# Performance work log

Measured on AMD Instinct MI355X. Metric: run time of the kernel, lower is better.

The kernel has to match this reference:

```python
import jax, jax.numpy as jnp
import numpy as np

D_MODEL = 1024
NHEAD = 16
HEAD_DIM = D_MODEL // NHEAD
EPS = 1e-5


def layer_norm(x, gamma, beta):
    mu = jnp.mean(x, axis=-1, keepdims=True)
    var = jnp.mean(jnp.square(x - mu), axis=-1, keepdims=True)
    return (x - mu) * jax.lax.rsqrt(var + EPS) * gamma + beta


def setup_inputs() -> dict:
    key = jax.random.key(0)
    ks = jax.random.split(key, 12)
    d = D_MODEL
    s = 1.0 / np.sqrt(d)
    return {
        "x": jax.random.normal(ks[0], (4, 2048, d), dtype=jnp.float32),
        "wq": jax.random.normal(ks[1], (d, d), dtype=jnp.float32) * s,
        "wk": jax.random.normal(ks[2], (d, d), dtype=jnp.float32) * s,
        "wv": jax.random.normal(ks[3], (d, d), dtype=jnp.float32) * s,
        "wo": jax.random.normal(ks[4], (d, d), dtype=jnp.float32) * s,
        "bo": jnp.zeros((d,), dtype=jnp.float32),
        "gx": jnp.ones((d,), dtype=jnp.float32),
        "bx": jnp.zeros((d,), dtype=jnp.float32),
        "gf": jnp.ones((d,), dtype=jnp.float32),
        "bf": jnp.zeros((d,), dtype=jnp.float32),
        "w1": jax.random.normal(ks[5], (d, d), dtype=jnp.float32) * s,
        "b1": jnp.zeros((d,), dtype=jnp.float32),
        "w2": jax.random.normal(ks[6], (d, d), dtype=jnp.float32) * s,
        "b2": jnp.zeros((d,), dtype=jnp.float32),
    }


def reference(x, wq, wk, wv, wo, bo, gx, bx, gf, bf, w1, b1, w2, b2):
    B, S, D = x.shape
    H, Dh = NHEAD, HEAD_DIM
    xs = layer_norm(x, gx, bx)
    q = (xs @ wq).reshape(B, S, H, Dh)
    k = (xs @ wk).reshape(B, S, H, Dh)
    v = (xs @ wv).reshape(B, S, H, Dh)
    scores = jnp.einsum("bqhd,bkhd->bhqk", q, k) / jnp.sqrt(jnp.float32(Dh))
    attn = jax.nn.softmax(scores, axis=-1)  # dropout p=0 -> identity
    o = jnp.einsum("bhqk,bkhd->bqhd", attn, v).reshape(B, S, D)
    attn_out = o @ wo + bo
    xt = x + attn_out
    h = layer_norm(xt, gf, bf)
    ffn = jax.nn.relu(h @ w1 + b1) @ w2 + b2
    return xt + ffn
```

## Files before the change

### kernel.cpp

```cpp
#include <hip/hip_runtime.h>
#include <hip/hip_bf16.h>

typedef __bf16 bf16;
typedef bf16 bf16x8 __attribute__((ext_vector_type(8)));
typedef bf16 bf16x4 __attribute__((ext_vector_type(4)));
typedef float f32x4 __attribute__((ext_vector_type(4)));
typedef float f32x16 __attribute__((ext_vector_type(16)));

#define AS1 __attribute__((address_space(1)))
#define AS3 __attribute__((address_space(3)))

static constexpr int SEQ = 2048;
static constexpr int NH  = 16;
static constexpr int DH  = 64;
static constexpr float SCLQ = 0.125f * 1.44269504088896340736f;

__device__ __forceinline__ void gload16(const void* g, void* l) {
  __builtin_amdgcn_global_load_lds((const AS1 void*)g, (AS3 void*)l, 16, 0, 0);
}

__device__ __forceinline__ unsigned pk2(float a, float b) {
  union { bf16 h[2]; unsigned u; } z;
  z.h[0] = (bf16)a; z.h[1] = (bf16)b;
  return z.u;
}

__device__ __forceinline__ void plswap(unsigned &a, unsigned &b) {
  asm volatile("v_permlane32_swap_b32 %0, %1" : "+v"(a), "+v"(b));
}

__global__ __launch_bounds__(256) void prep_w(
    const float* __restrict__ w0, const float* __restrict__ w1,
    const float* __restrict__ w2, const float* __restrict__ w3,
    const float* __restrict__ w4, const float* __restrict__ w5,
    bf16* __restrict__ dst)
{
  __shared__ float tile[64][65];
  int bid = blockIdx.x;
  int wi = bid >> 8;
  int tl = bid & 255;
  int tk = (tl >> 4) << 6;
  int tn = (tl & 15) << 6;
  const float* W = w0;
  if (wi == 1) W = w1; else if (wi == 2) W = w2; else if (wi == 3) W = w3;
  else if (wi == 4) W = w4; else if (wi == 5) W = w5;
  int t = threadIdx.x;
  #pragma unroll
  for (int rep = 0; rep < 16; ++rep) {
    int idx = rep * 256 + t;
    int i = idx >> 6, j = idx & 63;
    tile[i][j] = W[(size_t)(tk + i) * 1024 + tn + j];
  }
  __syncthreads();
  bf16* out = dst + (size_t)wi * 1024 * 1024;
  #pragma unroll
  for (int rep = 0; rep < 16; ++rep) {
    int idx = rep * 256 + t;
    int i = idx >> 6, j = idx & 63;
    out[(size_t)(tn + i) * 1024 + tk + j] = (bf16)tile[j][i];
  }
}

__global__ __launch_bounds__(256) void ln_k(
    const float* __restrict__ x, const float* __restrict__ g,
    const float* __restrict__ bb, bf16* __restrict__ out)
{
  int row = blockIdx.x;
  int t = threadIdx.x;
  float4 v = ((const float4*)(x + (size_t)row * 1024))[t];
  float s  = v.x + v.y + v.z + v.w;
  float s2 = v.x * v.x + v.y * v.y + v.z * v.z + v.w * v.w;
  #pragma unroll
  for (int m = 1; m < 64; m <<= 1) { s += __shfl_xor(s, m); s2 += __shfl_xor(s2, m); }
  __shared__ float red[8];
  int w = t >> 6;
  if ((t & 63) == 0) { red[w] = s; red[4 + w] = s2; }
  __syncthreads();
  s  = red[0] + red[1] + red[2] + red[3];
  s2 = red[4] + red[5] + red[6] + red[7];
  float mu  = s * (1.0f / 1024.0f);
  float var = s2 * (1.0f / 1024.0f) - mu * mu;
  float rst = rsqrtf(var + 1e-5f);
  float4 gv = ((const float4*)g)[t];
  float4 bv = ((const float4*)bb)[t];
  bf16x4 o;
  o[0] = (bf16)((v.x - mu) * rst * gv.x + bv.x);
  o[1] = (bf16)((v.y - mu) * rst * gv.y + bv.y);
  o[2] = (bf16)((v.z - mu) * rst * gv.z + bv.z);
  o[3] = (bf16)((v.w - mu) * rst * gv.w + bv.w);
  *(bf16x4*)(out + (size_t)row * 1024 + t * 4) = o;
}

template<int EPI, int NT>
__global__ __launch_bounds__(256) void gemm_k(
    const bf16* __restrict__ A, const bf16* __restrict__ Bt,
    const float* __restrict__ bias, const float* __restrict__ res,
    float* __restrict__ outf, bf16* __restrict__ outb)
{
  __shared__ bf16 lA[128 * 64];
  __shared__ bf16 lB[128 * 64];
  int t = threadIdx.x;
  int wg = blockIdx.x;
  int swz = (wg & 7) * (NT * 8) + (wg >> 3);
  int mt = swz / NT, nt = swz % NT;
  int lane = t & 63, w = t >> 6;
  int l16 = lane & 15, lh = lane >> 4;
  int wr = w >> 1, wc = w & 1;

  f32x4 acc[4][4] = {};
  const size_t mbase = (size_t)mt * 128;
  const size_t nbase = (size_t)nt * 128;
  int u = t & 7;

  for (int ks = 0; ks < 16; ++ks) {
    int k0 = ks * 64;
    #pragma unroll
    for (int i = 0; i < 4; ++i) {
      int row = i * 32 + (t >> 3);
      int up = u ^ (row & 7);
      gload16(A  + (mbase + row) * 1024 + k0 + up * 8, lA + i * 2048 + w * 512);
      gload16(Bt + (nbase + row) * 1024 + k0 + up * 8, lB + i * 2048 + w * 512);
    }
    __syncthreads();
    #pragma unroll
    for (int kc = 0; kc < 2; ++kc) {
      bf16x8 af[4], bfr[4];
      #pragma unroll
      for (int mi = 0; mi < 4; ++mi) {
        int row = wr * 64 + mi * 16 + l16;
        af[mi] = *(const bf16x8*)(lA + row * 64 + (((kc * 4 + lh) ^ (row & 7)) * 8));
      }
      #pragma unroll
      for (int ni = 0; ni < 4; ++ni) {
        int row = wc * 64 + ni * 16 + l16;
        bfr[ni] = *(const bf16x8*)(lB + row * 64 + (((kc * 4 + lh) ^ (row & 7)) * 8));
      }
      #pragma unroll
      for (int mi = 0; mi < 4; ++mi)
        #pragma unroll
        for (int ni = 0; ni < 4; ++ni)
          acc[mi][ni] = __builtin_amdgcn_mfma_f32_16x16x32_bf16(af[mi], bfr[ni], acc[mi][ni], 0, 0, 0);
    }
    __syncthreads();
  }

  int mrow0 = mt * 128 + wr * 64;
  int ncol0 = nt * 128 + wc * 64;
  #pragma unroll
  for (int mi = 0; mi < 4; ++mi) {
    #pragma unroll
    for (int ni = 0; ni < 4; ++ni) {
      if constexpr (EPI == 0) {
        int gcol = ncol0 + ni * 16 + l16;
        int which = gcol >> 10;
        int col = gcol & 1023;
        int h = col >> 6, dh = col & 63;
        bf16* dst = outb + (size_t)which * (size_t)(4 * NH * SEQ * DH);
        if (which == 2) {
          int s0 = mrow0 + mi * 16 + lh * 4;
          int b = s0 >> 11, s = s0 & 2047;
          bf16x4 pkv;
          #pragma unroll
          for (int r = 0; r < 4; ++r) pkv[r] = (bf16)acc[mi][ni][r];
          *(bf16x4*)(dst + (((size_t)((b * NH + h) * DH + dh)) << 11) + s) = pkv;
        } else {
          #pragma unroll
          for (int r = 0; r < 4; ++r) {
            int grow = mrow0 + mi * 16 + lh * 4 + r;
            int b = grow >> 11, s = grow & 2047;
            float v = acc[mi][ni][r];
            if (which == 0) v *= SCLQ;
            dst[(((size_t)((b * NH + h) * SEQ + s)) << 6) + dh] = (bf16)v;
          }
        }
      } else {
        #pragma unroll
        for (int r = 0; r < 4; ++r) {
          int grow = mrow0 + mi * 16 + lh * 4 + r;
          int gcol = ncol0 + ni * 16 + l16;
          float v = acc[mi][ni][r];
          if constexpr (EPI == 2) {
            size_t idx = (size_t)grow * 1024 + gcol;
            outf[idx] = v + bias[gcol] + res[idx];
          } else {
            size_t idx = (size_t)grow * 1024 + gcol;
            float z = v + bias[gcol];
            outb[idx] = (bf16)(z > 0.f ? z : 0.f);
          }
        }
      }
    }
  }
}

__global__ __launch_bounds__(256) void attn_k(
    const bf16* __restrict__ q, const bf16* __restrict__ kk,
    const bf16* __restrict__ vt, bf16* __restrict__ o)
{
  __shared__ bf16 lK[2][4096];
  __shared__ bf16 lV[2][4096];

  int t = threadIdx.x;
  int lane = t & 63, w = t >> 6;
  int l31 = lane & 31, hi = lane >> 5;
  int bid = blockIdx.x;
  int swz = (bid & 7) * 128 + (bid >> 3);
  int bh = swz >> 4, qt = swz & 15;
  int q0 = qt * 128 + w * 32;
  size_t bhS = (size_t)bh * SEQ;

  const bf16* qrow = q + (bhS + q0 + l31) * 64 + hi * 8;
  bf16x8 aq[4];
  #pragma unroll
  for (int ks = 0; ks < 4; ++ks) aq[ks] = *(const bf16x8*)(qrow + ks * 16);

  int srow = t >> 3;
  int u8 = (t & 7) ^ (srow & 7);
  const bf16* kSrc = kk + (bhS + srow) * 64 + u8 * 8;
  const bf16* vSrc = vt + ((size_t)bh * 64 + srow) * SEQ + u8 * 8;

  f32x16 oacc[2] = {};
  float lsum = 0.f;

  gload16(kSrc,            &lK[0][w * 512]);
  gload16(kSrc + 2048,     &lK[0][2048 + w * 512]);
  gload16(vSrc,            &lV[0][w * 512]);
  gload16(vSrc + 32 * SEQ, &lV[0][2048 + w * 512]);
  __syncthreads();

  #pragma unroll 2
  for (int kt = 0; kt < 32; ++kt) {
    const int cur = kt & 1;
    if (kt < 31) {
      const bf16* ks2 = kSrc + (size_t)(kt + 1) * 4096;
      const bf16* vs2 = vSrc + (kt + 1) * 64;
      gload16(ks2,            &lK[cur ^ 1][w * 512]);
      gload16(ks2 + 2048,     &lK[cur ^ 1][2048 + w * 512]);
      gload16(vs2,            &lV[cur ^ 1][w * 512]);
      gload16(vs2 + 32 * SEQ, &lV[cur ^ 1][2048 + w * 512]);
    }

    const bf16* bK = &lK[cur][0];
    const bf16* bV = &lV[cur][0];

    f32x16 sA = {}, sB = {};
    __builtin_amdgcn_s_setprio(1);
    #pragma unroll
    for (int ks = 0; ks < 4; ++ks) {
      int u = ((2 * ks + hi) ^ (l31 & 7)) * 8;
      bf16x8 k0 = *(const bf16x8*)(bK + l31 * 64 + u);
      bf16x8 k1 = *(const bf16x8*)(bK + (32 + l31) * 64 + u);
      sA = __builtin_amdgcn_mfma_f32_32x32x16_bf16(k0, aq[ks], sA, 0, 0, 0);
      sB = __builtin_amdgcn_mfma_f32_32x32x16_bf16(k1, aq[ks], sB, 0, 0, 0);
    }
    __builtin_amdgcn_s_setprio(0);

    float p[32];
    #pragma unroll
    for (int i = 0; i < 16; ++i) {
      p[i]      = __builtin_amdgcn_exp2f(sA[i]);
      p[16 + i] = __builtin_amdgcn_exp2f(sB[i]);
    }

    float t8[8];
    #pragma unroll
    for (int i = 0; i < 8; ++i)
      t8[i] = (p[4 * i] + p[4 * i + 1]) + (p[4 * i + 2] + p[4 * i + 3]);
    lsum += ((t8[0] + t8[1]) + (t8[2] + t8[3])) + ((t8[4] + t8[5]) + (t8[6] + t8[7]));

    __builtin_amdgcn_s_setprio(1);
    #pragma unroll
    for (int ks = 0; ks < 4; ++ks) {
      int g = 8 * ks;
      unsigned X0 = pk2(p[g],     p[g + 1]), X1 = pk2(p[g + 2], p[g + 3]);
      unsigned Y0 = pk2(p[g + 4], p[g + 5]), Y1 = pk2(p[g + 6], p[g + 7]);
      plswap(X0, Y0);
      plswap(X1, Y1);
      union { unsigned u[4]; bf16x8 v; } cv;
      cv.u[0] = X0; cv.u[1] = X1; cv.u[2] = Y0; cv.u[3] = Y1;
      int u = ((2 * ks + hi) ^ (l31 & 7)) * 8;
      bf16x8 v0 = *(const bf16x8*)(bV + l31 * 64 + u);
      bf16x8 v1 = *(const bf16x8*)(bV + (32 + l31) * 64 + u);
      oacc[0] = __builtin_amdgcn_mfma_f32_32x32x16_bf16(cv.v, v0, oacc[0], 0, 0, 0);
      oacc[1] = __builtin_amdgcn_mfma_f32_32x32x16_bf16(cv.v, v1, oacc[1], 0, 0, 0);
    }
    __builtin_amdgcn_s_setprio(0);

    __syncthreads();
  }

  lsum += __shfl_xor(lsum, 32);
  float inv = 1.0f / lsum;
  int bb = bh >> 4, hh = bh & 15;
  size_t obase = ((size_t)bb * SEQ + q0) * 1024 + (size_t)hh * 64;
  #pragma unroll
  for (int r = 0; r < 16; ++r) {
    int qrw = (r & 3) + 8 * (r >> 2) + 4 * hi;
    float iv = __shfl(inv, qrw);
    size_t base = obase + (size_t)qrw * 1024;
    o[base + l31]      = (bf16)(oacc[0][r] * iv);
    o[base + 32 + l31] = (bf16)(oacc[1][r] * iv);
  }
}

extern "C" void kernel_launch(void* const* d_in, const int* in_sizes, int n_in,
                              void* d_out, int out_size, void* d_ws, size_t ws_size,
                              hipStream_t stream) {
  const float* x   = (const float*)d_in[0];
  const float* wq  = (const float*)d_in[1];
  const float* wk  = (const float*)d_in[2];
  const float* wv  = (const float*)d_in[3];
  const float* wo  = (const float*)d_in[4];
  const float* bo  = (const float*)d_in[5];
  const float* gx  = (const float*)d_in[6];
  const float* bx  = (const float*)d_in[7];
  const float* gf  = (const float*)d_in[8];
  const float* bfp = (const float*)d_in[9];
  const float* w1  = (const float*)d_in[10];
  const float* b1  = (const float*)d_in[11];
  const float* w2  = (const float*)d_in[12];
  const float* b2  = (const float*)d_in[13];

  char* ws = (char*)d_ws;
  const size_t MB = 1024 * 1024;
  bf16*  wT  = (bf16*)ws;
  bf16*  xs  = (bf16*)(ws + 12 * MB);
  bf16*  qb  = (bf16*)(ws + 28 * MB);
  bf16*  kb  = (bf16*)(ws + 44 * MB);
  bf16*  vtb = (bf16*)(ws + 60 * MB);
  bf16*  ob  = (bf16*)(ws + 12 * MB);
  float* xt  = (float*)(ws + 28 * MB);
  bf16*  hb  = (bf16*)(ws + 60 * MB);
  bf16*  a1  = (bf16*)(ws + 12 * MB);
  float* out = (float*)d_out;

  prep_w<<<1536, 256, 0, stream>>>(wq, wk, wv, wo, w1, w2, wT);
  ln_k<<<8192, 256, 0, stream>>>(x, gx, bx, xs);
  gemm_k<0, 24><<<1536, 256, 0, stream>>>(xs, wT, nullptr, nullptr, nullptr, qb);
  attn_k<<<1024, 256, 0, stream>>>(qb, kb, vtb, ob);
  gemm_k<2, 8><<<512, 256, 0, stream>>>(ob, wT + (size_t)3 * MB, bo, x, xt, nullptr);
  ln_k<<<8192, 256, 0, stream>>>(xt, gf, bfp, hb);
  gemm_k<3, 8><<<512, 256, 0, stream>>>(hb, wT + (size_t)4 * MB, b1, nullptr, nullptr, a1);
  gemm_k<2, 8><<<512, 256, 0, stream>>>(a1, wT + (size_t)5 * MB, b2, xt, out, nullptr);
}
```

Before: 292.0 us.

## Double-buffer GEMM LDS tiles with 256x128 tiles and 8-wave ping-pong schedule

Rewrites the GEMM main loop to use 512-thread blocks computing 256x128 output tiles, with double-buffered LDS so the next K slice loads while MFMAs run on the current one. Global-to-LDS loads are split into chunks placed between MFMA groups, and s_setprio raises priority during the MFMA bursts in a barrier-synchronised ping-pong. Grid sizes and the tile swizzle are halved to match. This raises LDS use and adds many barriers per iteration, and fewer blocks could reduce occupancy on the smaller GEMMs.

```diff
diff --git a/kernel.cpp b/kernel.cpp
--- a/kernel.cpp
+++ b/kernel.cpp
@@ -28,6 +28,8 @@
 __device__ __forceinline__ void plswap(unsigned &a, unsigned &b) {
   asm volatile("v_permlane32_swap_b32 %0, %1" : "+v"(a), "+v"(b));
 }
+
+#define MFMA16(d, a, b) d = __builtin_amdgcn_mfma_f32_16x16x32_bf16(a, b, d, 0, 0, 0)
 
 __global__ __launch_bounds__(256) void prep_w(
     const float* __restrict__ w0, const float* __restrict__ w1,
@@ -92,59 +94,120 @@
 }
 
 template<int EPI, int NT>
-__global__ __launch_bounds__(256) void gemm_k(
+__global__ __launch_bounds__(512) void gemm_k(
     const bf16* __restrict__ A, const bf16* __restrict__ Bt,
     const float* __restrict__ bias, const float* __restrict__ res,
     float* __restrict__ outf, bf16* __restrict__ outb)
 {
-  __shared__ bf16 lA[128 * 64];
-  __shared__ bf16 lB[128 * 64];
+  __shared__ bf16 lA[2][256 * 64];
+  __shared__ bf16 lB[2][128 * 64];
   int t = threadIdx.x;
   int wg = blockIdx.x;
-  int swz = (wg & 7) * (NT * 8) + (wg >> 3);
+  int swz = (wg & 7) * (NT * 4) + (wg >> 3);
   int mt = swz / NT, nt = swz % NT;
   int lane = t & 63, w = t >> 6;
   int l16 = lane & 15, lh = lane >> 4;
   int wr = w >> 1, wc = w & 1;
 
   f32x4 acc[4][4] = {};
-  const size_t mbase = (size_t)mt * 128;
-  const size_t nbase = (size_t)nt * 128;
-  int u = t & 7;
+
+  const int trow = t >> 3;
+  const int up = (t & 7) ^ (trow & 7);
+  const bf16* aSrc = A  + ((size_t)mt * 256 + trow) * 1024 + up * 8;
+  const bf16* bSrc = Bt + ((size_t)nt * 128 + trow) * 1024 + up * 8;
+  const int ldsOff = w * 512;
+
+  #pragma unroll
+  for (int c = 0; c < 4; ++c) gload16(aSrc + c * 65536, &lA[0][c * 4096 + ldsOff]);
+  #pragma unroll
+  for (int c = 0; c < 2; ++c) gload16(bSrc + c * 65536, &lB[0][c * 4096 + ldsOff]);
+  asm volatile("s_waitcnt vmcnt(0)" ::: "memory");
+  __builtin_amdgcn_s_barrier();
+
+  const int ar0 = (wr * 64 + l16) * 64;
+  const int br0 = (wc * 64 + l16) * 64;
+  const int x7 = l16 & 7;
+  const int u0 = (lh ^ x7) * 8;
+  const int u1 = ((4 + lh) ^ x7) * 8;
 
   for (int ks = 0; ks < 16; ++ks) {
-    int k0 = ks * 64;
-    #pragma unroll
-    for (int i = 0; i < 4; ++i) {
-      int row = i * 32 + (t >> 3);
-      int up = u ^ (row & 7);
-      gload16(A  + (mbase + row) * 1024 + k0 + up * 8, lA + i * 2048 + w * 512);
-      gload16(Bt + (nbase + row) * 1024 + k0 + up * 8, lB + i * 2048 + w * 512);
-    }
-    __syncthreads();
-    #pragma unroll
-    for (int kc = 0; kc < 2; ++kc) {
-      bf16x8 af[4], bfr[4];
-      #pragma unroll
-      for (int mi = 0; mi < 4; ++mi) {
-        int row = wr * 64 + mi * 16 + l16;
-        af[mi] = *(const bf16x8*)(lA + row * 64 + (((kc * 4 + lh) ^ (row & 7)) * 8));
-      }
-      #pragma unroll
-      for (int ni = 0; ni < 4; ++ni) {
-        int row = wc * 64 + ni * 16 + l16;
-        bfr[ni] = *(const bf16x8*)(lB + row * 64 + (((kc * 4 + lh) ^ (row & 7)) * 8));
-      }
-      #pragma unroll
-      for (int mi = 0; mi < 4; ++mi)
-        #pragma unroll
-        for (int ni = 0; ni < 4; ++ni)
-          acc[mi][ni] = __builtin_amdgcn_mfma_f32_16x16x32_bf16(af[mi], bfr[ni], acc[mi][ni], 0, 0, 0);
-    }
-    __syncthreads();
-  }
-
-  int mrow0 = mt * 128 + wr * 64;
+    const int cur = ks & 1;
+    const bf16* bufA = &lA[cur][0];
+    const bf16* bufB = &lB[cur][0];
+    bf16* nA = &lA[cur ^ 1][0];
+    bf16* nB = &lB[cur ^ 1][0];
+    const int k1 = (ks + 1) * 64;
+    const bool pf = (ks < 15);
+
+    bf16x8 af0, af1, bfr[4];
+
+    bfr[0] = *(const bf16x8*)(bufB + br0 +        u0);
+    bfr[1] = *(const bf16x8*)(bufB + br0 + 1024 + u0);
+    bfr[2] = *(const bf16x8*)(bufB + br0 + 2048 + u0);
+    bfr[3] = *(const bf16x8*)(bufB + br0 + 3072 + u0);
+    af0    = *(const bf16x8*)(bufA + ar0 +        u0);
+    af1    = *(const bf16x8*)(bufA + ar0 + 1024 + u0);
+    if (pf) {
+      gload16(aSrc + k1,         nA + ldsOff);
+      gload16(aSrc + k1 + 65536, nA + 4096 + ldsOff);
+    }
+    __builtin_amdgcn_s_barrier();
+    __builtin_amdgcn_s_setprio(1);
+    MFMA16(acc[0][0], af0, bfr[0]); MFMA16(acc[0][1], af0, bfr[1]);
+    MFMA16(acc[0][2], af0, bfr[2]); MFMA16(acc[0][3], af0, bfr[3]);
+    MFMA16(acc[1][0], af1, bfr[0]); MFMA16(acc[1][1], af1, bfr[1]);
+    MFMA16(acc[1][2], af1, bfr[2]); MFMA16(acc[1][3], af1, bfr[3]);
+    __builtin_amdgcn_s_setprio(0);
+    __builtin_amdgcn_s_barrier();
+
+    af0 = *(const bf16x8*)(bufA + ar0 + 2048 + u0);
+    af1 = *(const bf16x8*)(bufA + ar0 + 3072 + u0);
+    if (pf) {
+      gload16(aSrc + k1 + 131072, nA + 8192  + ldsOff);
+      gload16(aSrc + k1 + 196608, nA + 12288 + ldsOff);
+    }
+    __builtin_amdgcn_s_barrier();
+    __builtin_amdgcn_s_setprio(1);
+    MFMA16(acc[2][0], af0, bfr[0]); MFMA16(acc[2][1], af0, bfr[1]);
+    MFMA16(acc[2][2], af0, bfr[2]); MFMA16(acc[2][3], af0, bfr[3]);
+    MFMA16(acc[3][0], af1, bfr[0]); MFMA16(acc[3][1], af1, bfr[1]);
+    MFMA16(acc[3][2], af1, bfr[2]); MFMA16(acc[3][3], af1, bfr[3]);
+    __builtin_amdgcn_s_setprio(0);
+    __builtin_amdgcn_s_barrier();
+
+    bfr[0] = *(const bf16x8*)(bufB + br0 +        u1);
+    bfr[1] = *(const bf16x8*)(bufB + br0 + 1024 + u1);
+    bfr[2] = *(const bf16x8*)(bufB + br0 + 2048 + u1);
+    bfr[3] = *(const bf16x8*)(bufB + br0 + 3072 + u1);
+    af0    = *(const bf16x8*)(bufA + ar0 +        u1);
+    af1    = *(const bf16x8*)(bufA + ar0 + 1024 + u1);
+    if (pf) {
+      gload16(bSrc + k1,         nB + ldsOff);
+      gload16(bSrc + k1 + 65536, nB + 4096 + ldsOff);
+    }
+    __builtin_amdgcn_s_barrier();
+    __builtin_amdgcn_s_setprio(1);
+    MFMA16(acc[0][0], af0, bfr[0]); MFMA16(acc[0][1], af0, bfr[1]);
+    MFMA16(acc[0][2], af0, bfr[2]); MFMA16(acc[0][3], af0, bfr[3]);
+    MFMA16(acc[1][0], af1, bfr[0]); MFMA16(acc[1][1], af1, bfr[1]);
+    MFMA16(acc[1][2], af1, bfr[2]); MFMA16(acc[1][3], af1, bfr[3]);
+    __builtin_amdgcn_s_setprio(0);
+    __builtin_amdgcn_s_barrier();
+
+    af0 = *(const bf16x8*)(bufA + ar0 + 2048 + u1);
+    af1 = *(const bf16x8*)(bufA + ar0 + 3072 + u1);
+    __builtin_amdgcn_s_barrier();
+    __builtin_amdgcn_s_setprio(1);
+    MFMA16(acc[2][0], af0, bfr[0]); MFMA16(acc[2][1], af0, bfr[1]);
+    MFMA16(acc[2][2], af0, bfr[2]); MFMA16(acc[2][3], af0, bfr[3]);
+    MFMA16(acc[3][0], af1, bfr[0]); MFMA16(acc[3][1], af1, bfr[1]);
+    MFMA16(acc[3][2], af1, bfr[2]); MFMA16(acc[3][3], af1, bfr[3]);
+    __builtin_amdgcn_s_setprio(0);
+    asm volatile("s_waitcnt vmcnt(0)" ::: "memory");
+    __builtin_amdgcn_s_barrier();
+  }
+
+  int mrow0 = mt * 256 + wr * 64;
   int ncol0 = nt * 128 + wc * 64;
   #pragma unroll
   for (int mi = 0; mi < 4; ++mi) {
@@ -336,10 +399,10 @@
 
   prep_w<<<1536, 256, 0, stream>>>(wq, wk, wv, wo, w1, w2, wT);
   ln_k<<<8192, 256, 0, stream>>>(x, gx, bx, xs);
-  gemm_k<0, 24><<<1536, 256, 0, stream>>>(xs, wT, nullptr, nullptr, nullptr, qb);
+  gemm_k<0, 24><<<768, 512, 0, stream>>>(xs, wT, nullptr, nullptr, nullptr, qb);
   attn_k<<<1024, 256, 0, stream>>>(qb, kb, vtb, ob);
-  gemm_k<2, 8><<<512, 256, 0, stream>>>(ob, wT + (size_t)3 * MB, bo, x, xt, nullptr);
+  gemm_k<2, 8><<<256, 512, 0, stream>>>(ob, wT + (size_t)3 * MB, bo, x, xt, nullptr);
   ln_k<<<8192, 256, 0, stream>>>(xt, gf, bfp, hb);
-  gemm_k<3, 8><<<512, 256, 0, stream>>>(hb, wT + (size_t)4 * MB, b1, nullptr, nullptr, a1);
-  gemm_k<2, 8><<<512, 256, 0, stream>>>(a1, wT + (size_t)5 * MB, b2, xt, out, nullptr);
-}
+  gemm_k<3, 8><<<256, 512, 0, stream>>>(hb, wT + (size_t)4 * MB, b1, nullptr, nullptr, a1);
+  gemm_k<2, 8><<<256, 512, 0, stream>>>(a1, wT + (size_t)5 * MB, b2, xt, out, nullptr);
+}
```

Measured after the change: 312.4 us. +7.0%, slower.

## Split attention key tile into two 32-key halves to cut registers

Applied to the files above, without the earlier changes.

The attention inner loop now handles the 64-key tile as two sequential 32-key halves, each doing QK^T, exp2, row-sum and its share of the PV MFMAs. This shrinks live registers (one 16-wide score accumulator and 16 probabilities at a time instead of 32), and the launch bounds now request 4 blocks per CU to target higher occupancy. In exchange, the QK and PV MFMAs lose some independence, which may reduce instruction-level overlap within a wave.

```diff
diff --git a/kernel.cpp b/kernel.cpp
--- a/kernel.cpp
+++ b/kernel.cpp
@@ -28,6 +28,8 @@
 __device__ __forceinline__ void plswap(unsigned &a, unsigned &b) {
   asm volatile("v_permlane32_swap_b32 %0, %1" : "+v"(a), "+v"(b));
 }
+
+#define MFMA32(d, a, b) d = __builtin_amdgcn_mfma_f32_32x32x16_bf16(a, b, d, 0, 0, 0)
 
 __global__ __launch_bounds__(256) void prep_w(
     const float* __restrict__ w0, const float* __restrict__ w1,
@@ -193,7 +195,7 @@
   }
 }
 
-__global__ __launch_bounds__(256) void attn_k(
+__global__ __launch_bounds__(256, 4) void attn_k(
     const bf16* __restrict__ q, const bf16* __restrict__ kk,
     const bf16* __restrict__ vt, bf16* __restrict__ o)
 {
@@ -219,7 +221,7 @@
   const bf16* kSrc = kk + (bhS + srow) * 64 + u8 * 8;
   const bf16* vSrc = vt + ((size_t)bh * 64 + srow) * SEQ + u8 * 8;
 
-  f32x16 oacc[2] = {};
+  f32x16 oa0 = {}, oa1 = {};
   float lsum = 0.f;
 
   gload16(kSrc,            &lK[0][w * 512]);
@@ -243,48 +245,88 @@
     const bf16* bK = &lK[cur][0];
     const bf16* bV = &lV[cur][0];
 
-    f32x16 sA = {}, sB = {};
-    __builtin_amdgcn_s_setprio(1);
-    #pragma unroll
-    for (int ks = 0; ks < 4; ++ks) {
-      int u = ((2 * ks + hi) ^ (l31 & 7)) * 8;
-      bf16x8 k0 = *(const bf16x8*)(bK + l31 * 64 + u);
-      bf16x8 k1 = *(const bf16x8*)(bK + (32 + l31) * 64 + u);
-      sA = __builtin_amdgcn_mfma_f32_32x32x16_bf16(k0, aq[ks], sA, 0, 0, 0);
-      sB = __builtin_amdgcn_mfma_f32_32x32x16_bf16(k1, aq[ks], sB, 0, 0, 0);
-    }
-    __builtin_amdgcn_s_setprio(0);
-
-    float p[32];
-    #pragma unroll
-    for (int i = 0; i < 16; ++i) {
-      p[i]      = __builtin_amdgcn_exp2f(sA[i]);
-      p[16 + i] = __builtin_amdgcn_exp2f(sB[i]);
-    }
-
-    float t8[8];
-    #pragma unroll
-    for (int i = 0; i < 8; ++i)
-      t8[i] = (p[4 * i] + p[4 * i + 1]) + (p[4 * i + 2] + p[4 * i + 3]);
-    lsum += ((t8[0] + t8[1]) + (t8[2] + t8[3])) + ((t8[4] + t8[5]) + (t8[6] + t8[7]));
-
-    __builtin_amdgcn_s_setprio(1);
-    #pragma unroll
-    for (int ks = 0; ks < 4; ++ks) {
-      int g = 8 * ks;
-      unsigned X0 = pk2(p[g],     p[g + 1]), X1 = pk2(p[g + 2], p[g + 3]);
-      unsigned Y0 = pk2(p[g + 4], p[g + 5]), Y1 = pk2(p[g + 6], p[g + 7]);
-      plswap(X0, Y0);
-      plswap(X1, Y1);
-      union { unsigned u[4]; bf16x8 v; } cv;
-      cv.u[0] = X0; cv.u[1] = X1; cv.u[2] = Y0; cv.u[3] = Y1;
-      int u = ((2 * ks + hi) ^ (l31 & 7)) * 8;
-      bf16x8 v0 = *(const bf16x8*)(bV + l31 * 64 + u);
-      bf16x8 v1 = *(const bf16x8*)(bV + (32 + l31) * 64 + u);
-      oacc[0] = __builtin_amdgcn_mfma_f32_32x32x16_bf16(cv.v, v0, oacc[0], 0, 0, 0);
-      oacc[1] = __builtin_amdgcn_mfma_f32_32x32x16_bf16(cv.v, v1, oacc[1], 0, 0, 0);
-    }
-    __builtin_amdgcn_s_setprio(0);
+    {
+      f32x16 s = {};
+      __builtin_amdgcn_s_setprio(1);
+      #pragma unroll
+      for (int ks = 0; ks < 4; ++ks) {
+        int u = ((2 * ks + hi) ^ (l31 & 7)) * 8;
+        bf16x8 k0 = *(const bf16x8*)(bK + l31 * 64 + u);
+        MFMA32(s, k0, aq[ks]);
+      }
+      __builtin_amdgcn_s_setprio(0);
+      float p[16];
+      #pragma unroll
+      for (int i = 0; i < 16; ++i) p[i] = __builtin_amdgcn_exp2f(s[i]);
+      float t8[4];
+      #pragma unroll
+      for (int i = 0; i < 4; ++i)
+        t8[i] = (p[4 * i] + p[4 * i + 1]) + (p[4 * i + 2] + p[4 * i + 3]);
+      lsum += (t8[0] + t8[1]) + (t8[2] + t8[3]);
+      unsigned cv[2][4];
+      #pragma unroll
+      for (int g2 = 0; g2 < 2; ++g2) {
+        int g = 8 * g2;
+        unsigned X0 = pk2(p[g],     p[g + 1]), X1 = pk2(p[g + 2], p[g + 3]);
+        unsigned Y0 = pk2(p[g + 4], p[g + 5]), Y1 = pk2(p[g + 6], p[g + 7]);
+        plswap(X0, Y0); plswap(X1, Y1);
+        cv[g2][0] = X0; cv[g2][1] = X1; cv[g2][2] = Y0; cv[g2][3] = Y1;
+      }
+      __builtin_amdgcn_s_setprio(1);
+      #pragma unroll
+      for (int ks = 0; ks < 2; ++ks) {
+        int u = ((2 * ks + hi) ^ (l31 & 7)) * 8;
+        bf16x8 v0 = *(const bf16x8*)(bV + l31 * 64 + u);
+        bf16x8 v1 = *(const bf16x8*)(bV + (32 + l31) * 64 + u);
+        union { unsigned u4[4]; bf16x8 v; } a;
+        a.u4[0] = cv[ks][0]; a.u4[1] = cv[ks][1]; a.u4[2] = cv[ks][2]; a.u4[3] = cv[ks][3];
+        MFMA32(oa0, a.v, v0);
+        MFMA32(oa1, a.v, v1);
+      }
+      __builtin_amdgcn_s_setprio(0);
+    }
+
+    {
+      f32x16 s = {};
+      __builtin_amdgcn_s_setprio(1);
+      #pragma unroll
+      for (int ks = 0; ks < 4; ++ks) {
+        int u = ((2 * ks + hi) ^ (l31 & 7)) * 8;
+        bf16x8 k1 = *(const bf16x8*)(bK + (32 + l31) * 64 + u);
+        MFMA32(s, k1, aq[ks]);
+      }
+      __builtin_amdgcn_s_setprio(0);
+      float p[16];
+      #pragma unroll
+      for (int i = 0; i < 16; ++i) p[i] = __builtin_amdgcn_exp2f(s[i]);
+      float t8[4];
+      #pragma unroll
+      for (int i = 0; i < 4; ++i)
+        t8[i] = (p[4 * i] + p[4 * i + 1]) + (p[4 * i + 2] + p[4 * i + 3]);
+      lsum += (t8[0] + t8[1]) + (t8[2] + t8[3]);
+      unsigned cv[2][4];
+      #pragma unroll
+      for (int g2 = 0; g2 < 2; ++g2) {
+        int g = 8 * g2;
+        unsigned X0 = pk2(p[g],     p[g + 1]), X1 = pk2(p[g + 2], p[g + 3]);
+        unsigned Y0 = pk2(p[g + 4], p[g + 5]), Y1 = pk2(p[g + 6], p[g + 7]);
+        plswap(X0, Y0); plswap(X1, Y1);
+        cv[g2][0] = X0; cv[g2][1] = X1; cv[g2][2] = Y0; cv[g2][3] = Y1;
+      }
+      __builtin_amdgcn_s_setprio(1);
+      #pragma unroll
+      for (int ks = 2; ks < 4; ++ks) {
+        int u = ((2 * ks + hi) ^ (l31 & 7)) * 8;
+        bf16x8 v0 = *(const bf16x8*)(bV + l31 * 64 + u);
+        bf16x8 v1 = *(const bf16x8*)(bV + (32 + l31) * 64 + u);
+        union { unsigned u4[4]; bf16x8 v; } a;
+        a.u4[0] = cv[ks - 2][0]; a.u4[1] = cv[ks - 2][1];
+        a.u4[2] = cv[ks - 2][2]; a.u4[3] = cv[ks - 2][3];
+        MFMA32(oa0, a.v, v0);
+        MFMA32(oa1, a.v, v1);
+      }
+      __builtin_amdgcn_s_setprio(0);
+    }
 
     __syncthreads();
   }
@@ -298,8 +340,8 @@
     int qrw = (r & 3) + 8 * (r >> 2) + 4 * hi;
     float iv = __shfl(inv, qrw);
     size_t base = obase + (size_t)qrw * 1024;
-    o[base + l31]      = (bf16)(oacc[0][r] * iv);
-    o[base + 32 + l31] = (bf16)(oacc[1][r] * iv);
+    o[base + l31]      = (bf16)(oa0[r] * iv);
+    o[base + 32 + l31] = (bf16)(oa1[r] * iv);
   }
 }
 
```

After: 281.0 us. 1.04x faster.
